# Kernel tuning notes

Measured on AMD Instinct MI355X. Metric: run time of the kernel, lower is better.

## Reference

```python
import jax, jax.numpy as jnp
import numpy as np

HEADS = 12
EPS_RMS = 1e-6
EPS_LN = 1e-5


def _rms_inorm(x, w):
    # torch.std over spatial dims (unbiased, ddof=1); no mean subtraction
    std = jnp.std(x, axis=(2, 3), keepdims=True, ddof=1)
    return x / (std + EPS_RMS) * w[None, :, None, None]


def _layernorm(x, w, b):
    m = jnp.mean(x, axis=-1, keepdims=True)
    v = jnp.var(x, axis=-1, keepdims=True)
    return (x - m) / jnp.sqrt(v + EPS_LN) * w + b


def setup_inputs() -> dict:
    key = jax.random.key(0)
    ks = jax.random.split(key, 16)
    B, C, H, W = 8, 768, 64, 64
    hd = C // HEADS
    s = 0.02
    return {
        "x": jax.random.normal(ks[0], (B, C, H, W), jnp.float32),
        "bcs": jnp.zeros((1, 2), jnp.int32),
        "norm1_w": jnp.ones((C,), jnp.float32),
        "norm2_w": jnp.ones((C,), jnp.float32),
        "mlpn_w": jnp.ones((C,), jnp.float32),
        "Win": jax.random.normal(ks[1], (3 * C, C), jnp.float32) * s,
        "bin_": jnp.zeros((3 * C,), jnp.float32),
        "Wout": jax.random.normal(ks[2], (C, C), jnp.float32) * s,
        "bout": jnp.zeros((C,), jnp.float32),
        "qn_w": jnp.ones((hd,), jnp.float32),
        "qn_b": jnp.zeros((hd,), jnp.float32),
        "kn_w": jnp.ones((hd,), jnp.float32),
        "kn_b": jnp.zeros((hd,), jnp.float32),
        "gamma_att": jnp.full((C,), 1e-6, jnp.float32),
        "gamma_mlp": jnp.full((C,), 1e-6, jnp.float32),
        "W1": jax.random.normal(ks[3], (C, 4 * C), jnp.float32) * s,
        "b1": jnp.zeros((4 * C,), jnp.float32),
        "W2": jax.random.normal(ks[4], (4 * C, C), jnp.float32) * s,
        "b2": jnp.zeros((C,), jnp.float32),
    }


def reference(x, bcs, norm1_w, norm2_w, mlpn_w, Win, bin_, Wout, bout,
              qn_w, qn_b, kn_w, kn_b, gamma_att, gamma_mlp, W1, b1, W2, b2):
    B, C, H, W = x.shape
    hd = C // HEADS
    scale = 1.0 / jnp.sqrt(jnp.asarray(hd, x.dtype))

    h = _rms_inorm(x, norm1_w)
    # 1x1 conv QKV: [B, 3C, H, W]
    qkv = jnp.einsum('bchw,oc->bohw', h, Win) + bin_[None, :, None, None]
    # b (he c3) h w -> b he h w c3, then split into q,k,v of head_dim each
    qkv = qkv.reshape(B, HEADS, 3 * hd, H, W).transpose(0, 1, 3, 4, 2)
    q, k, v = jnp.split(qkv, 3, axis=-1)  # each [B, he, H, W, hd]
    q = _layernorm(q, qn_w, qn_b)
    k = _layernorm(k, kn_w, kn_b)

    # row attention: attend along W for each row h
    sx = jnp.einsum('bnhqc,bnhkc->bnhqk', q, k) * scale
    xx = jnp.einsum('bnhqk,bnhkc->bnhqc', jax.nn.softmax(sx, axis=-1), v)
    # column attention: attend along H for each column w
    sy = jnp.einsum('bnqwc,bnkwc->bnwqk', q, k) * scale
    xy = jnp.einsum('bnwqk,bnkwc->bnqwc', jax.nn.softmax(sy, axis=-1), v)

    a = (xx + xy) * 0.5  # [B, he, H, W, hd]
    a = a.transpose(0, 1, 4, 2, 3).reshape(B, C, H, W)
    a = _rms_inorm(a, norm2_w)
    a = jnp.einsum('bchw,oc->bohw', a, Wout) + bout[None, :, None, None]
    x1 = a * gamma_att[None, :, None, None] + x

    t = x1.transpose(0, 2, 3, 1)  # [B, H, W, C]
    m = jax.nn.gelu(t @ W1 + b1, approximate=False) @ W2 + b2
    m = m.transpose(0, 3, 1, 2)
    m = _rms_inorm(m, mlpn_w)
    return x1 + gamma_mlp[None, :, None, None] * m
```

## Files before the change

kernel.cpp:

```cpp
#include <hip/hip_runtime.h>

typedef __attribute__((ext_vector_type(8))) short short8;
typedef __attribute__((ext_vector_type(4))) float f32x4;
typedef __attribute__((ext_vector_type(4))) unsigned short u16x4;
typedef __attribute__((ext_vector_type(8))) unsigned short u16x8;

#define BDIM 8
#define CDIM 768
#define C3 2304
#define C4 3072
#define HEADS 12
#define HD 64
#define HWD 4096
#define TOKS 32768

__device__ __forceinline__ float bf2f(unsigned short u) {
    union { unsigned int i; float f; } x; x.i = ((unsigned int)u) << 16; return x.f;
}
__device__ __forceinline__ unsigned short f2bf(float f) {
    union { float f; unsigned int i; } x; x.f = f;
    unsigned int r = x.i + 0x7FFFu + ((x.i >> 16) & 1u);
    return (unsigned short)(r >> 16);
}

__device__ __forceinline__ void gload_lds16(const unsigned short* g, unsigned short* l) {
    __builtin_amdgcn_global_load_lds(
        (const __attribute__((address_space(1))) void*)g,
        (__attribute__((address_space(3))) void*)l, 16, 0, 0);
}

__global__ __launch_bounds__(256) void convert_f32_bf16(
    const float* __restrict__ src, unsigned short* __restrict__ dst, int n)
{
    int i = (blockIdx.x * 256 + threadIdx.x) * 4;
    if (i + 3 >= n + 4) return;
    if (i + 3 < n) {
        float4 v = *(const float4*)&src[i];
        dst[i + 0] = f2bf(v.x); dst[i + 1] = f2bf(v.y);
        dst[i + 2] = f2bf(v.z); dst[i + 3] = f2bf(v.w);
    }
}

__global__ __launch_bounds__(256) void transpose_w(
    const float* __restrict__ src, unsigned short* __restrict__ dst, int R, int Cc)
{
    const int n0 = blockIdx.x * 64, k0 = blockIdx.y * 64;
    __shared__ float t[64][65];
    #pragma unroll
    for (int s = 0; s < 16; ++s) {
        int flat = threadIdx.x + 256 * s;
        int i = flat >> 6, j = flat & 63;
        t[i][j] = src[(long)(k0 + i) * Cc + n0 + j];
    }
    __syncthreads();
    #pragma unroll
    for (int s = 0; s < 16; ++s) {
        int flat = threadIdx.x + 256 * s;
        int jn = flat >> 6, ik = flat & 63;
        dst[(long)(n0 + jn) * R + k0 + ik] = f2bf(t[ik][jn]);
    }
}

__global__ __launch_bounds__(256) void stats_spatial_f32(
    const float* __restrict__ x, const float* __restrict__ wgt,
    float* __restrict__ sout, float eps)
{
    const int bc = blockIdx.x;
    const int c = bc % CDIM;
    const float4* p4 = (const float4*)(x + (long)bc * HWD);
    float s = 0.f, ss = 0.f;
    #pragma unroll
    for (int k = 0; k < 4; ++k) {
        float4 v = p4[threadIdx.x + 256 * k];
        s  += v.x + v.y + v.z + v.w;
        ss += v.x * v.x + v.y * v.y + v.z * v.z + v.w * v.w;
    }
    #pragma unroll
    for (int m = 1; m < 64; m <<= 1) { s += __shfl_xor(s, m); ss += __shfl_xor(ss, m); }
    __shared__ float rs[4], rss[4];
    int w = threadIdx.x >> 6, lane = threadIdx.x & 63;
    if (lane == 0) { rs[w] = s; rss[w] = ss; }
    __syncthreads();
    if (threadIdx.x == 0) {
        float S = rs[0] + rs[1] + rs[2] + rs[3];
        float Q = rss[0] + rss[1] + rss[2] + rss[3];
        float var = (Q - S * S * (1.f / 4096.f)) * (1.f / 4095.f);
        sout[bc] = wgt[c] / (sqrtf(var) + eps);
    }
}

__global__ __launch_bounds__(256) void stats_spatial_bf16(
    const unsigned short* __restrict__ t, const float* __restrict__ wgt,
    float* __restrict__ sout, float eps)
{
    const int b = blockIdx.x / 12, cg = blockIdx.x % 12;
    const int sub = threadIdx.x & 15, tr = threadIdx.x >> 4;
    const unsigned short* base = t + (long)b * HWD * CDIM + cg * 64 + sub * 4;
    float s[4] = {0.f, 0.f, 0.f, 0.f}, q[4] = {0.f, 0.f, 0.f, 0.f};
    for (int i = 0; i < 256; ++i) {
        const int token = tr + 16 * i;
        u16x4 v = *(const u16x4*)(base + (long)token * CDIM);
        #pragma unroll
        for (int j = 0; j < 4; ++j) { float f = bf2f(v[j]); s[j] += f; q[j] += f * f; }
    }
    __shared__ float ssum[16][64], ssq[16][64];
    #pragma unroll
    for (int j = 0; j < 4; ++j) { ssum[tr][sub * 4 + j] = s[j]; ssq[tr][sub * 4 + j] = q[j]; }
    __syncthreads();
    if (threadIdx.x < 64) {
        const int c = threadIdx.x;
        float S = 0.f, Q = 0.f;
        #pragma unroll
        for (int r = 0; r < 16; ++r) { S += ssum[r][c]; Q += ssq[r][c]; }
        const float var = (Q - S * S * (1.f / 4096.f)) * (1.f / 4095.f);
        const int cglob = cg * 64 + c;
        sout[b * CDIM + cglob] = wgt[cglob] / (sqrtf(var) + eps);
    }
}

__global__ __launch_bounds__(256) void make_h(
    const float* __restrict__ x, const float* __restrict__ s1,
    unsigned short* __restrict__ h)
{
    const int hw0 = blockIdx.x * 64, c0 = blockIdx.y * 64, b = blockIdx.z;
    __shared__ float t[64][65];
    #pragma unroll
    for (int s = 0; s < 16; ++s) {
        int flat = threadIdx.x + 256 * s;
        int ci = flat >> 6, hj = flat & 63;
        t[ci][hj] = x[(long)(b * CDIM + c0 + ci) * HWD + hw0 + hj];
    }
    __syncthreads();
    #pragma unroll
    for (int s = 0; s < 16; ++s) {
        int flat = threadIdx.x + 256 * s;
        int hi = flat >> 6, cj = flat & 63;
        float v = t[cj][hi] * s1[b * CDIM + c0 + cj];
        h[(long)(b * HWD + hw0 + hi) * CDIM + c0 + cj] = f2bf(v);
    }
}

template<int GELU>
__global__ __launch_bounds__(512, 2) void gemm256(
    const unsigned short* __restrict__ A, const unsigned short* __restrict__ BT,
    const float* __restrict__ bias, unsigned short* __restrict__ out,
    int M, int N, int K)
{
    extern __shared__ unsigned short smem[];
    const int tid = threadIdx.x;
    const int lane = tid & 63, w = tid >> 6;
    const int wm = w >> 2, wn = w & 3;
    const int lr = lane & 15, g = lane >> 4;

    const int nwg = gridDim.x;
    const int logical = (blockIdx.x & 7) * (nwg >> 3) + (blockIdx.x >> 3);
    const int gnx = N >> 8;
    const int n0 = (logical % gnx) << 8;
    const int m0 = (logical / gnx) << 8;

    const int ka = (((tid & 3) ^ ((tid >> 3) & 3)) << 3);
    const int rA0 = tid >> 2, rA1 = (512 + tid) >> 2;
    const unsigned short* aS0 = A + (long)(m0 + rA0) * K + ka;
    const unsigned short* aS1 = A + (long)(m0 + rA1) * K + ka;
    const unsigned short* bS0 = BT + (long)(n0 + rA0) * K + ka;
    const unsigned short* bS1 = BT + (long)(n0 + rA1) * K + ka;
    unsigned short* dA0 = smem + ((tid & ~63) + 0) * 8;
    unsigned short* dA1 = smem + ((tid & ~63) + 512) * 8;
    unsigned short* dB0 = dA0 + 32768;
    unsigned short* dB1 = dA1 + 32768;

#define GSTAGE(S) do { \
        gload_lds16(aS0, dA0 + (S) * 8192); \
        gload_lds16(aS1, dA1 + (S) * 8192); \
        gload_lds16(bS0, dB0 + (S) * 8192); \
        gload_lds16(bS1, dB1 + (S) * 8192); \
        aS0 += 32; aS1 += 32; bS0 += 32; bS1 += 32; } while (0)

    const int nsub = K >> 5;
    const int koff = ((g ^ ((lr >> 1) & 3)) << 3);
    const unsigned short* baseA = smem + (wm * 128 + lr) * 32 + koff;
    const unsigned short* baseB = smem + 32768 + (wn * 64 + lr) * 32 + koff;

    f32x4 acc[8][4] = {};

    GSTAGE(0); GSTAGE(1); GSTAGE(2);
    asm volatile("s_waitcnt vmcnt(8)" ::: "memory");
    __builtin_amdgcn_s_barrier();

#define FRAGS_AND_MFMA(U) do { \
        short8 bf[4], af[8]; \
        _Pragma("unroll") \
        for (int ni = 0; ni < 4; ++ni) bf[ni] = *(const short8*)(baseB + (U) * 8192 + ni * 512); \
        _Pragma("unroll") \
        for (int mi = 0; mi < 8; ++mi) af[mi] = *(const short8*)(baseA + (U) * 8192 + mi * 512); \
        STAGE_##U; \
        __builtin_amdgcn_s_setprio(1); \
        _Pragma("unroll") \
        for (int mi = 0; mi < 8; ++mi) \
            _Pragma("unroll") \
            for (int ni = 0; ni < 4; ++ni) \
                acc[mi][ni] = __builtin_amdgcn_mfma_f32_16x16x32_bf16(af[mi], bf[ni], acc[mi][ni], 0, 0, 0); \
        __builtin_amdgcn_s_setprio(0); \
        WAIT_##U; \
        __builtin_amdgcn_s_barrier(); \
        __builtin_amdgcn_sched_barrier(0); } while (0)

    int j4 = 0;
    for (; j4 + 4 < nsub; j4 += 4) {
#define STAGE_0 GSTAGE(3)
#define STAGE_1 GSTAGE(0)
#define STAGE_2 GSTAGE(1)
#define STAGE_3 GSTAGE(2)
#define WAIT_0 asm volatile("s_waitcnt vmcnt(8)" ::: "memory")
#define WAIT_1 asm volatile("s_waitcnt vmcnt(8)" ::: "memory")
#define WAIT_2 asm volatile("s_waitcnt vmcnt(8)" ::: "memory")
#define WAIT_3 asm volatile("s_waitcnt vmcnt(8)" ::: "memory")
        FRAGS_AND_MFMA(0);
        FRAGS_AND_MFMA(1);
        FRAGS_AND_MFMA(2);
        FRAGS_AND_MFMA(3);
#undef STAGE_0
#undef STAGE_1
#undef STAGE_2
#undef STAGE_3
#undef WAIT_0
#undef WAIT_1
#undef WAIT_2
#undef WAIT_3
    }
    {
#define STAGE_0 GSTAGE(3)
#define STAGE_1
#define STAGE_2
#define STAGE_3
#define WAIT_0 asm volatile("s_waitcnt vmcnt(8)" ::: "memory")
#define WAIT_1 asm volatile("s_waitcnt vmcnt(4)" ::: "memory")
#define WAIT_2 asm volatile("s_waitcnt vmcnt(0)" ::: "memory")
#define WAIT_3
        FRAGS_AND_MFMA(0);
        FRAGS_AND_MFMA(1);
        FRAGS_AND_MFMA(2);
        FRAGS_AND_MFMA(3);
#undef STAGE_0
#undef STAGE_1
#undef STAGE_2
#undef STAGE_3
#undef WAIT_0
#undef WAIT_1
#undef WAIT_2
#undef WAIT_3
    }
#undef FRAGS_AND_MFMA
#undef GSTAGE

    #pragma unroll
    for (int mi = 0; mi < 8; ++mi) {
        #pragma unroll
        for (int ni = 0; ni < 4; ++ni) {
            const int gcol = n0 + wn * 64 + ni * 16 + lr;
            const float bv = bias[gcol];
            #pragma unroll
            for (int r = 0; r < 4; ++r) {
                const int grow = m0 + wm * 128 + mi * 16 + g * 4 + r;
                float v = acc[mi][ni][r] + bv;
                if (GELU) v = 0.5f * v * (1.f + erff(v * 0.70710678118f));
                out[(long)grow * N + gcol] = f2bf(v);
            }
        }
    }
}

__global__ __launch_bounds__(256) void qk_layernorm(
    unsigned short* __restrict__ qkv,
    const float* __restrict__ qw, const float* __restrict__ qb,
    const float* __restrict__ kw, const float* __restrict__ kb)
{
    const int pairIdx = blockIdx.x * 16 + (threadIdx.x >> 4);
    const int token = pairIdx / HEADS, he = pairIdx % HEADS;
    const int c4 = (threadIdx.x & 15) * 4;
    const long base = (long)token * C3 + he * 192;
    #pragma unroll
    for (int which = 0; which < 2; ++which) {
        const long off = base + which * 64 + c4;
        u16x4 v = *(u16x4*)&qkv[off];
        float f[4];
        #pragma unroll
        for (int j = 0; j < 4; ++j) f[j] = bf2f(v[j]);
        float s = f[0] + f[1] + f[2] + f[3];
        float q = f[0] * f[0] + f[1] * f[1] + f[2] * f[2] + f[3] * f[3];
        #pragma unroll
        for (int m = 1; m < 16; m <<= 1) { s += __shfl_xor(s, m); q += __shfl_xor(q, m); }
        const float mean = s * (1.f / 64.f);
        const float var = q * (1.f / 64.f) - mean * mean;
        const float rstd = rsqrtf(var + 1e-5f);
        const float* W = which ? kw : qw;
        const float* Bv = which ? kb : qb;
        u16x4 o;
        #pragma unroll
        for (int j = 0; j < 4; ++j)
            o[j] = f2bf((f[j] - mean) * rstd * W[c4 + j] + Bv[c4 + j]);
        *(u16x4*)&qkv[off] = o;
    }
}

template<int AXIS>
__global__ __launch_bounds__(128) void attn_axial(
    const unsigned short* __restrict__ qkv, unsigned short* __restrict__ a)
{
    __shared__ unsigned short lds[2][2][64 * 72];
    const int tid = threadIdx.x;
    const int lane = tid & 63, w = tid >> 6;
    const int lineG = blockIdx.x * 2 + w;
    const int b = lineG / 768;
    const int rem = lineG - b * 768;
    const int he = rem >> 6, line = rem & 63;
    const int ts = (AXIS == 0) ? 1 : 64;
    const long token0 = (long)b * HWD + (AXIS == 0 ? line * 64 : line);
    const long qbase = token0 * C3 + he * 192;
    unsigned short* VT = &lds[w][0][0];
    unsigned short* P  = &lds[w][1][0];
    const int lr = lane & 15, g = lane >> 4;

    {
        const int keyr = lane >> 3, d8 = (lane & 7) << 3;
        #pragma unroll
        for (int it = 0; it < 8; ++it) {
            const int key = it * 8 + keyr;
            u16x8 v = *(const u16x8*)&qkv[qbase + (long)key * ts * C3 + 128 + d8];
            #pragma unroll
            for (int j = 0; j < 8; ++j) VT[(d8 + j) * 72 + key] = v[j];
        }
    }

    short8 qf[4][2], kf[4][2];
    #pragma unroll
    for (int i = 0; i < 4; ++i)
        #pragma unroll
        for (int kk = 0; kk < 2; ++kk) {
            const long rb = qbase + (long)(i * 16 + lr) * ts * C3 + kk * 32 + g * 8;
            qf[i][kk] = *(const short8*)&qkv[rb];
            kf[i][kk] = *(const short8*)&qkv[rb + 64];
        }

    f32x4 acc[4][4] = {};
    #pragma unroll
    for (int mi = 0; mi < 4; ++mi)
        #pragma unroll
        for (int ni = 0; ni < 4; ++ni) {
            acc[mi][ni] = __builtin_amdgcn_mfma_f32_16x16x32_bf16(qf[mi][0], kf[ni][0], acc[mi][ni], 0, 0, 0);
            acc[mi][ni] = __builtin_amdgcn_mfma_f32_16x16x32_bf16(qf[mi][1], kf[ni][1], acc[mi][ni], 0, 0, 0);
        }

    #pragma unroll
    for (int mi = 0; mi < 4; ++mi)
        #pragma unroll
        for (int r = 0; r < 4; ++r) {
            float mx = -1e30f;
            #pragma unroll
            for (int ni = 0; ni < 4; ++ni) {
                float v = acc[mi][ni][r] * 0.125f; acc[mi][ni][r] = v; mx = fmaxf(mx, v);
            }
            #pragma unroll
            for (int m = 1; m < 16; m <<= 1) mx = fmaxf(mx, __shfl_xor(mx, m));
            float s = 0.f;
            #pragma unroll
            for (int ni = 0; ni < 4; ++ni) {
                float e = __expf(acc[mi][ni][r] - mx); acc[mi][ni][r] = e; s += e;
            }
            #pragma unroll
            for (int m = 1; m < 16; m <<= 1) s += __shfl_xor(s, m);
            const float inv = 1.f / s;
            const int row = mi * 16 + 4 * g + r;
            #pragma unroll
            for (int ni = 0; ni < 4; ++ni)
                P[row * 72 + ni * 16 + lr] = f2bf(acc[mi][ni][r] * inv);
        }
    __syncthreads();

    short8 pa[4][2], vb[4][2];
    #pragma unroll
    for (int i = 0; i < 4; ++i)
        #pragma unroll
        for (int kk = 0; kk < 2; ++kk) {
            pa[i][kk] = *(const short8*)&P[(i * 16 + lr) * 72 + kk * 32 + g * 8];
            vb[i][kk] = *(const short8*)&VT[(i * 16 + lr) * 72 + kk * 32 + g * 8];
        }
    f32x4 o2[4][4] = {};
    #pragma unroll
    for (int mi = 0; mi < 4; ++mi)
        #pragma unroll
        for (int ni = 0; ni < 4; ++ni) {
            o2[mi][ni] = __builtin_amdgcn_mfma_f32_16x16x32_bf16(pa[mi][0], vb[ni][0], o2[mi][ni], 0, 0, 0);
            o2[mi][ni] = __builtin_amdgcn_mfma_f32_16x16x32_bf16(pa[mi][1], vb[ni][1], o2[mi][ni], 0, 0, 0);
        }

    #pragma unroll
    for (int mi = 0; mi < 4; ++mi)
        #pragma unroll
        for (int r = 0; r < 4; ++r) {
            const int q = mi * 16 + 4 * g + r;
            const long tok = token0 + (long)q * ts;
            #pragma unroll
            for (int ni = 0; ni < 4; ++ni) {
                const int d = ni * 16 + lr;
                const long addr = tok * CDIM + he * 64 + d;
                const float v = o2[mi][ni][r] * 0.5f;
                if (AXIS == 0) a[addr] = f2bf(v);
                else           a[addr] = f2bf(bf2f(a[addr]) + v);
            }
        }
}

__global__ __launch_bounds__(256) void scale_inplace(
    unsigned short* __restrict__ a, const float* __restrict__ s2)
{
    const long i = ((long)blockIdx.x * 256 + threadIdx.x) * 4;
    const int c = (int)(i % CDIM);
    const int b = (int)(i / ((long)CDIM * HWD));
    u16x4 v = *(u16x4*)&a[i];
    u16x4 o;
    #pragma unroll
    for (int j = 0; j < 4; ++j) o[j] = f2bf(bf2f(v[j]) * s2[b * CDIM + c + j]);
    *(u16x4*)&a[i] = o;
}

__global__ __launch_bounds__(256) void x1_combine(
    const unsigned short* __restrict__ o, const float* __restrict__ x,
    const float* __restrict__ gamma, float* __restrict__ dout,
    unsigned short* __restrict__ x1b)
{
    const int hw0 = blockIdx.x * 64, c0 = blockIdx.y * 64, b = blockIdx.z;
    __shared__ float t[64][65];
    #pragma unroll
    for (int s = 0; s < 16; ++s) {
        int flat = threadIdx.x + 256 * s;
        int i = flat >> 6, j = flat & 63;
        t[i][j] = bf2f(o[(long)(b * HWD + hw0 + i) * CDIM + c0 + j]);
    }
    __syncthreads();
    #pragma unroll
    for (int s = 0; s < 16; ++s) {
        int flat = threadIdx.x + 256 * s;
        int j = flat >> 6, i = flat & 63;
        const long xi = (long)(b * CDIM + c0 + j) * HWD + hw0 + i;
        float v = x[xi] + gamma[c0 + j] * t[i][j];
        dout[xi] = v;
        t[i][j] = v;
    }
    __syncthreads();
    #pragma unroll
    for (int s = 0; s < 16; ++s) {
        int flat = threadIdx.x + 256 * s;
        int i = flat >> 6, j = flat & 63;
        x1b[(long)(b * HWD + hw0 + i) * CDIM + c0 + j] = f2bf(t[i][j]);
    }
}

__global__ __launch_bounds__(256) void final_combine(
    const unsigned short* __restrict__ m, const float* __restrict__ gm,
    const float* __restrict__ s3, float* __restrict__ dout)
{
    const int hw0 = blockIdx.x * 64, c0 = blockIdx.y * 64, b = blockIdx.z;
    __shared__ float t[64][65];
    #pragma unroll
    for (int s = 0; s < 16; ++s) {
        int flat = threadIdx.x + 256 * s;
        int i = flat >> 6, j = flat & 63;
        t[i][j] = bf2f(m[(long)(b * HWD + hw0 + i) * CDIM + c0 + j]);
    }
    __syncthreads();
    #pragma unroll
    for (int s = 0; s < 16; ++s) {
        int flat = threadIdx.x + 256 * s;
        int j = flat >> 6, i = flat & 63;
        const long xi = (long)(b * CDIM + c0 + j) * HWD + hw0 + i;
        dout[xi] = dout[xi] + gm[c0 + j] * s3[b * CDIM + c0 + j] * t[i][j];
    }
}

extern "C" void kernel_launch(void* const* d_in, const int* in_sizes, int n_in,
                              void* d_out, int out_size, void* d_ws, size_t ws_size,
                              hipStream_t stream) {
    const float* x      = (const float*)d_in[0];
    const float* n1w    = (const float*)d_in[2];
    const float* n2w    = (const float*)d_in[3];
    const float* mlw    = (const float*)d_in[4];
    const float* Win    = (const float*)d_in[5];
    const float* bin    = (const float*)d_in[6];
    const float* Wout   = (const float*)d_in[7];
    const float* bout   = (const float*)d_in[8];
    const float* qn_w   = (const float*)d_in[9];
    const float* qn_b   = (const float*)d_in[10];
    const float* kn_w   = (const float*)d_in[11];
    const float* kn_b   = (const float*)d_in[12];
    const float* gatt   = (const float*)d_in[13];
    const float* gmlp   = (const float*)d_in[14];
    const float* W1     = (const float*)d_in[15];
    const float* b1     = (const float*)d_in[16];
    const float* W2     = (const float*)d_in[17];
    const float* b2     = (const float*)d_in[18];
    float* dout = (float*)d_out;
    char* ws = (char*)d_ws;

    unsigned short* wQ  = (unsigned short*)(ws);
    unsigned short* wO  = (unsigned short*)(ws + (4L << 20));
    unsigned short* w1t = (unsigned short*)(ws + (6L << 20));
    unsigned short* w2t = (unsigned short*)(ws + (11L << 20));
    float* s1 = (float*)(ws + (16L << 20));
    float* s2 = s1 + 6144;
    float* s3 = s2 + 6144;
    unsigned short* bufH = (unsigned short*)(ws + (17L << 20));
    unsigned short* bufQ = (unsigned short*)(ws + (65L << 20));
    unsigned short* bufA = (unsigned short*)(ws + (209L << 20));

    hipFuncSetAttribute((const void*)&gemm256<0>, hipFuncAttributeMaxDynamicSharedMemorySize, 131072);
    hipFuncSetAttribute((const void*)&gemm256<1>, hipFuncAttributeMaxDynamicSharedMemorySize, 131072);

    convert_f32_bf16<<<1728, 256, 0, stream>>>(Win, wQ, C3 * CDIM);
    convert_f32_bf16<<<576, 256, 0, stream>>>(Wout, wO, CDIM * CDIM);
    transpose_w<<<dim3(C4 / 64, CDIM / 64), 256, 0, stream>>>(W1, w1t, CDIM, C4);
    transpose_w<<<dim3(CDIM / 64, C4 / 64), 256, 0, stream>>>(W2, w2t, C4, CDIM);

    stats_spatial_f32<<<BDIM * CDIM, 256, 0, stream>>>(x, n1w, s1, 1e-6f);
    make_h<<<dim3(64, 12, 8), 256, 0, stream>>>(x, s1, bufH);

    gemm256<0><<<(TOKS / 256) * (C3 / 256), 512, 131072, stream>>>(bufH, wQ, bin, bufQ, TOKS, C3, CDIM);
    qk_layernorm<<<TOKS * HEADS / 16, 256, 0, stream>>>(bufQ, qn_w, qn_b, kn_w, kn_b);

    attn_axial<0><<<BDIM * HEADS * 64 / 2, 128, 0, stream>>>(bufQ, bufA);
    attn_axial<1><<<BDIM * HEADS * 64 / 2, 128, 0, stream>>>(bufQ, bufA);

    stats_spatial_bf16<<<BDIM * 12, 256, 0, stream>>>(bufA, n2w, s2, 1e-6f);
    scale_inplace<<<TOKS * CDIM / 1024, 256, 0, stream>>>(bufA, s2);
    gemm256<0><<<(TOKS / 256) * (CDIM / 256), 512, 131072, stream>>>(bufA, wO, bout, bufH, TOKS, CDIM, CDIM);
    x1_combine<<<dim3(64, 12, 8), 256, 0, stream>>>(bufH, x, gatt, dout, bufA);

    for (int ch = 0; ch < 2; ++ch) {
        const unsigned short* x1c = bufA + (long)ch * 16384 * CDIM;
        unsigned short* mc = bufH + (long)ch * 16384 * CDIM;
        gemm256<1><<<(16384 / 256) * (C4 / 256), 512, 131072, stream>>>(x1c, w1t, b1, bufQ, 16384, C4, CDIM);
        gemm256<0><<<(16384 / 256) * (CDIM / 256), 512, 131072, stream>>>(bufQ, w2t, b2, mc, 16384, CDIM, C4);
    }

    stats_spatial_bf16<<<BDIM * 12, 256, 0, stream>>>(bufH, mlw, s3, 1e-6f);
    final_combine<<<dim3(64, 12, 8), 256, 0, stream>>>(bufH, gmlp, s3, dout);
}
```

Measured before the change: 972.8 us.

## Switch all projection and MLP GEMMs from bf16 to fp8 MFMA

Weights, normalized activations, the attention output, x1 and the GELU hidden activations are now quantized to fp8 instead of bf16. The GEMM kernel uses the fp8 16x16x32 MFMA, so operand bytes per element are halved. The LDS staging is reworked to one 16-byte load per thread per operand with an unswizzled layout, and the shared-memory footprint drops to 64 KB. The aim is to raise matrix-core throughput and cut memory traffic in the GEMM-dominated pipeline, at the cost of lower numerical accuracy in every projection.

```diff
diff --git a/kernel.cpp b/kernel.cpp
--- a/kernel.cpp
+++ b/kernel.cpp
@@ -22,27 +22,33 @@
     unsigned int r = x.i + 0x7FFFu + ((x.i >> 16) & 1u);
     return (unsigned short)(r >> 16);
 }
-
-__device__ __forceinline__ void gload_lds16(const unsigned short* g, unsigned short* l) {
+__device__ __forceinline__ unsigned char f2fp8(float v) {
+    return (unsigned char)(__builtin_amdgcn_cvt_pk_fp8_f32(v, v, 0, false) & 0xff);
+}
+__device__ __forceinline__ unsigned int f4fp8(float a, float b, float c, float d) {
+    int r = __builtin_amdgcn_cvt_pk_fp8_f32(a, b, 0, false);
+    r = __builtin_amdgcn_cvt_pk_fp8_f32(c, d, r, true);
+    return (unsigned int)r;
+}
+
+__device__ __forceinline__ void gload_lds16(const unsigned char* g, unsigned char* l) {
     __builtin_amdgcn_global_load_lds(
         (const __attribute__((address_space(1))) void*)g,
         (__attribute__((address_space(3))) void*)l, 16, 0, 0);
 }
 
-__global__ __launch_bounds__(256) void convert_f32_bf16(
-    const float* __restrict__ src, unsigned short* __restrict__ dst, int n)
+__global__ __launch_bounds__(256) void convert_f32_fp8(
+    const float* __restrict__ src, unsigned char* __restrict__ dst, int n)
 {
     int i = (blockIdx.x * 256 + threadIdx.x) * 4;
-    if (i + 3 >= n + 4) return;
     if (i + 3 < n) {
         float4 v = *(const float4*)&src[i];
-        dst[i + 0] = f2bf(v.x); dst[i + 1] = f2bf(v.y);
-        dst[i + 2] = f2bf(v.z); dst[i + 3] = f2bf(v.w);
-    }
-}
-
-__global__ __launch_bounds__(256) void transpose_w(
-    const float* __restrict__ src, unsigned short* __restrict__ dst, int R, int Cc)
+        *(unsigned int*)&dst[i] = f4fp8(v.x, v.y, v.z, v.w);
+    }
+}
+
+__global__ __launch_bounds__(256) void transpose_w_f8(
+    const float* __restrict__ src, unsigned char* __restrict__ dst, int R, int Cc)
 {
     const int n0 = blockIdx.x * 64, k0 = blockIdx.y * 64;
     __shared__ float t[64][65];
@@ -57,7 +63,7 @@
     for (int s = 0; s < 16; ++s) {
         int flat = threadIdx.x + 256 * s;
         int jn = flat >> 6, ik = flat & 63;
-        dst[(long)(n0 + jn) * R + k0 + ik] = f2bf(t[ik][jn]);
+        dst[(long)(n0 + jn) * R + k0 + ik] = f2fp8(t[ik][jn]);
     }
 }
 
@@ -120,7 +126,7 @@
 
 __global__ __launch_bounds__(256) void make_h(
     const float* __restrict__ x, const float* __restrict__ s1,
-    unsigned short* __restrict__ h)
+    unsigned char* __restrict__ h)
 {
     const int hw0 = blockIdx.x * 64, c0 = blockIdx.y * 64, b = blockIdx.z;
     __shared__ float t[64][65];
@@ -136,17 +142,17 @@
         int flat = threadIdx.x + 256 * s;
         int hi = flat >> 6, cj = flat & 63;
         float v = t[cj][hi] * s1[b * CDIM + c0 + cj];
-        h[(long)(b * HWD + hw0 + hi) * CDIM + c0 + cj] = f2bf(v);
-    }
-}
-
-template<int GELU>
+        h[(long)(b * HWD + hw0 + hi) * CDIM + c0 + cj] = f2fp8(v);
+    }
+}
+
+template<int GELU, int OUTF8>
 __global__ __launch_bounds__(512, 2) void gemm256(
-    const unsigned short* __restrict__ A, const unsigned short* __restrict__ BT,
-    const float* __restrict__ bias, unsigned short* __restrict__ out,
+    const unsigned char* __restrict__ A, const unsigned char* __restrict__ BT,
+    const float* __restrict__ bias, void* __restrict__ outv,
     int M, int N, int K)
 {
-    extern __shared__ unsigned short smem[];
+    extern __shared__ unsigned char smemB[];
     const int tid = threadIdx.x;
     const int lane = tid & 63, w = tid >> 6;
     const int wm = w >> 2, wn = w & 3;
@@ -158,48 +164,39 @@
     const int n0 = (logical % gnx) << 8;
     const int m0 = (logical / gnx) << 8;
 
-    const int ka = (((tid & 3) ^ ((tid >> 3) & 3)) << 3);
-    const int rA0 = tid >> 2, rA1 = (512 + tid) >> 2;
-    const unsigned short* aS0 = A + (long)(m0 + rA0) * K + ka;
-    const unsigned short* aS1 = A + (long)(m0 + rA1) * K + ka;
-    const unsigned short* bS0 = BT + (long)(n0 + rA0) * K + ka;
-    const unsigned short* bS1 = BT + (long)(n0 + rA1) * K + ka;
-    unsigned short* dA0 = smem + ((tid & ~63) + 0) * 8;
-    unsigned short* dA1 = smem + ((tid & ~63) + 512) * 8;
-    unsigned short* dB0 = dA0 + 32768;
-    unsigned short* dB1 = dA1 + 32768;
+    const unsigned char* aS = A + (long)(m0 + (tid >> 1)) * K + ((tid & 1) << 4);
+    const unsigned char* bS = BT + (long)(n0 + (tid >> 1)) * K + ((tid & 1) << 4);
+    unsigned char* dA = smemB + (tid & ~63) * 16;
+    unsigned char* dB = dA + 32768;
 
 #define GSTAGE(S) do { \
-        gload_lds16(aS0, dA0 + (S) * 8192); \
-        gload_lds16(aS1, dA1 + (S) * 8192); \
-        gload_lds16(bS0, dB0 + (S) * 8192); \
-        gload_lds16(bS1, dB1 + (S) * 8192); \
-        aS0 += 32; aS1 += 32; bS0 += 32; bS1 += 32; } while (0)
+        gload_lds16(aS, dA + (S) * 8192); \
+        gload_lds16(bS, dB + (S) * 8192); \
+        aS += 32; bS += 32; } while (0)
 
     const int nsub = K >> 5;
-    const int koff = ((g ^ ((lr >> 1) & 3)) << 3);
-    const unsigned short* baseA = smem + (wm * 128 + lr) * 32 + koff;
-    const unsigned short* baseB = smem + 32768 + (wn * 64 + lr) * 32 + koff;
+    const unsigned char* baseA = smemB + (wm * 128 + lr) * 32 + g * 8;
+    const unsigned char* baseB = smemB + 32768 + (wn * 64 + lr) * 32 + g * 8;
 
     f32x4 acc[8][4] = {};
 
     GSTAGE(0); GSTAGE(1); GSTAGE(2);
-    asm volatile("s_waitcnt vmcnt(8)" ::: "memory");
+    asm volatile("s_waitcnt vmcnt(4)" ::: "memory");
     __builtin_amdgcn_s_barrier();
 
 #define FRAGS_AND_MFMA(U) do { \
-        short8 bf[4], af[8]; \
+        long bf[4], af[8]; \
         _Pragma("unroll") \
-        for (int ni = 0; ni < 4; ++ni) bf[ni] = *(const short8*)(baseB + (U) * 8192 + ni * 512); \
+        for (int ni = 0; ni < 4; ++ni) bf[ni] = *(const long*)(baseB + (U) * 8192 + ni * 512); \
         _Pragma("unroll") \
-        for (int mi = 0; mi < 8; ++mi) af[mi] = *(const short8*)(baseA + (U) * 8192 + mi * 512); \
+        for (int mi = 0; mi < 8; ++mi) af[mi] = *(const long*)(baseA + (U) * 8192 + mi * 512); \
         STAGE_##U; \
         __builtin_amdgcn_s_setprio(1); \
         _Pragma("unroll") \
         for (int mi = 0; mi < 8; ++mi) \
             _Pragma("unroll") \
             for (int ni = 0; ni < 4; ++ni) \
-                acc[mi][ni] = __builtin_amdgcn_mfma_f32_16x16x32_bf16(af[mi], bf[ni], acc[mi][ni], 0, 0, 0); \
+                acc[mi][ni] = __builtin_amdgcn_mfma_f32_16x16x32_fp8_fp8(af[mi], bf[ni], acc[mi][ni], 0, 0, 0); \
         __builtin_amdgcn_s_setprio(0); \
         WAIT_##U; \
         __builtin_amdgcn_s_barrier(); \
@@ -211,10 +208,10 @@
 #define STAGE_1 GSTAGE(0)
 #define STAGE_2 GSTAGE(1)
 #define STAGE_3 GSTAGE(2)
-#define WAIT_0 asm volatile("s_waitcnt vmcnt(8)" ::: "memory")
-#define WAIT_1 asm volatile("s_waitcnt vmcnt(8)" ::: "memory")
-#define WAIT_2 asm volatile("s_waitcnt vmcnt(8)" ::: "memory")
-#define WAIT_3 asm volatile("s_waitcnt vmcnt(8)" ::: "memory")
+#define WAIT_0 asm volatile("s_waitcnt vmcnt(4)" ::: "memory")
+#define WAIT_1 asm volatile("s_waitcnt vmcnt(4)" ::: "memory")
+#define WAIT_2 asm volatile("s_waitcnt vmcnt(4)" ::: "memory")
+#define WAIT_3 asm volatile("s_waitcnt vmcnt(4)" ::: "memory")
         FRAGS_AND_MFMA(0);
         FRAGS_AND_MFMA(1);
         FRAGS_AND_MFMA(2);
@@ -233,8 +230,8 @@
 #define STAGE_1
 #define STAGE_2
 #define STAGE_3
-#define WAIT_0 asm volatile("s_waitcnt vmcnt(8)" ::: "memory")
-#define WAIT_1 asm volatile("s_waitcnt vmcnt(4)" ::: "memory")
+#define WAIT_0 asm volatile("s_waitcnt vmcnt(4)" ::: "memory")
+#define WAIT_1 asm volatile("s_waitcnt vmcnt(2)" ::: "memory")
 #define WAIT_2 asm volatile("s_waitcnt vmcnt(0)" ::: "memory")
 #define WAIT_3
         FRAGS_AND_MFMA(0);
@@ -264,7 +261,8 @@
                 const int grow = m0 + wm * 128 + mi * 16 + g * 4 + r;
                 float v = acc[mi][ni][r] + bv;
                 if (GELU) v = 0.5f * v * (1.f + erff(v * 0.70710678118f));
-                out[(long)grow * N + gcol] = f2bf(v);
+                if (OUTF8) ((unsigned char*)outv)[(long)grow * N + gcol] = f2fp8(v);
+                else       ((unsigned short*)outv)[(long)grow * N + gcol] = f2bf(v);
             }
         }
     }
@@ -411,23 +409,24 @@
         }
 }
 
-__global__ __launch_bounds__(256) void scale_inplace(
-    unsigned short* __restrict__ a, const float* __restrict__ s2)
+__global__ __launch_bounds__(256) void scale_convert(
+    const unsigned short* __restrict__ a, const float* __restrict__ s2,
+    unsigned char* __restrict__ aF)
 {
     const long i = ((long)blockIdx.x * 256 + threadIdx.x) * 4;
     const int c = (int)(i % CDIM);
     const int b = (int)(i / ((long)CDIM * HWD));
-    u16x4 v = *(u16x4*)&a[i];
-    u16x4 o;
-    #pragma unroll
-    for (int j = 0; j < 4; ++j) o[j] = f2bf(bf2f(v[j]) * s2[b * CDIM + c + j]);
-    *(u16x4*)&a[i] = o;
+    u16x4 v = *(const u16x4*)&a[i];
+    float f[4];
+    #pragma unroll
+    for (int j = 0; j < 4; ++j) f[j] = bf2f(v[j]) * s2[b * CDIM + c + j];
+    *(unsigned int*)&aF[i] = f4fp8(f[0], f[1], f[2], f[3]);
 }
 
 __global__ __launch_bounds__(256) void x1_combine(
     const unsigned short* __restrict__ o, const float* __restrict__ x,
     const float* __restrict__ gamma, float* __restrict__ dout,
-    unsigned short* __restrict__ x1b)
+    unsigned char* __restrict__ x1f)
 {
     const int hw0 = blockIdx.x * 64, c0 = blockIdx.y * 64, b = blockIdx.z;
     __shared__ float t[64][65];
@@ -452,7 +451,7 @@
     for (int s = 0; s < 16; ++s) {
         int flat = threadIdx.x + 256 * s;
         int i = flat >> 6, j = flat & 63;
-        x1b[(long)(b * HWD + hw0 + i) * CDIM + c0 + j] = f2bf(t[i][j]);
+        x1f[(long)(b * HWD + hw0 + i) * CDIM + c0 + j] = f2fp8(t[i][j]);
     }
 }
 
@@ -502,46 +501,46 @@
     float* dout = (float*)d_out;
     char* ws = (char*)d_ws;
 
-    unsigned short* wQ  = (unsigned short*)(ws);
-    unsigned short* wO  = (unsigned short*)(ws + (4L << 20));
-    unsigned short* w1t = (unsigned short*)(ws + (6L << 20));
-    unsigned short* w2t = (unsigned short*)(ws + (11L << 20));
-    float* s1 = (float*)(ws + (16L << 20));
+    unsigned char* wQf  = (unsigned char*)(ws);
+    unsigned char* wOf  = (unsigned char*)(ws + (2L << 20));
+    unsigned char* w1tf = (unsigned char*)(ws + (3L << 20));
+    unsigned char* w2tf = (unsigned char*)(ws + (6L << 20));
+    float* s1 = (float*)(ws + (9L << 20));
     float* s2 = s1 + 6144;
     float* s3 = s2 + 6144;
-    unsigned short* bufH = (unsigned short*)(ws + (17L << 20));
-    unsigned short* bufQ = (unsigned short*)(ws + (65L << 20));
-    unsigned short* bufA = (unsigned short*)(ws + (209L << 20));
-
-    hipFuncSetAttribute((const void*)&gemm256<0>, hipFuncAttributeMaxDynamicSharedMemorySize, 131072);
-    hipFuncSetAttribute((const void*)&gemm256<1>, hipFuncAttributeMaxDynamicSharedMemorySize, 131072);
-
-    convert_f32_bf16<<<1728, 256, 0, stream>>>(Win, wQ, C3 * CDIM);
-    convert_f32_bf16<<<576, 256, 0, stream>>>(Wout, wO, CDIM * CDIM);
-    transpose_w<<<dim3(C4 / 64, CDIM / 64), 256, 0, stream>>>(W1, w1t, CDIM, C4);
-    transpose_w<<<dim3(CDIM / 64, C4 / 64), 256, 0, stream>>>(W2, w2t, C4, CDIM);
+    unsigned char* R1 = (unsigned char*)(ws + (10L << 20));
+    unsigned short* R2 = (unsigned short*)(ws + (58L << 20));
+    unsigned short* R3 = (unsigned short*)(ws + (106L << 20));
+
+    hipFuncSetAttribute((const void*)&gemm256<0, 0>, hipFuncAttributeMaxDynamicSharedMemorySize, 65536);
+    hipFuncSetAttribute((const void*)&gemm256<1, 1>, hipFuncAttributeMaxDynamicSharedMemorySize, 65536);
+
+    convert_f32_fp8<<<1728, 256, 0, stream>>>(Win, wQf, C3 * CDIM);
+    convert_f32_fp8<<<576, 256, 0, stream>>>(Wout, wOf, CDIM * CDIM);
+    transpose_w_f8<<<dim3(C4 / 64, CDIM / 64), 256, 0, stream>>>(W1, w1tf, CDIM, C4);
+    transpose_w_f8<<<dim3(CDIM / 64, C4 / 64), 256, 0, stream>>>(W2, w2tf, C4, CDIM);
 
     stats_spatial_f32<<<BDIM * CDIM, 256, 0, stream>>>(x, n1w, s1, 1e-6f);
-    make_h<<<dim3(64, 12, 8), 256, 0, stream>>>(x, s1, bufH);
-
-    gemm256<0><<<(TOKS / 256) * (C3 / 256), 512, 131072, stream>>>(bufH, wQ, bin, bufQ, TOKS, C3, CDIM);
-    qk_layernorm<<<TOKS * HEADS / 16, 256, 0, stream>>>(bufQ, qn_w, qn_b, kn_w, kn_b);
-
-    attn_axial<0><<<BDIM * HEADS * 64 / 2, 128, 0, stream>>>(bufQ, bufA);
-    attn_axial<1><<<BDIM * HEADS * 64 / 2, 128, 0, stream>>>(bufQ, bufA);
-
-    stats_spatial_bf16<<<BDIM * 12, 256, 0, stream>>>(bufA, n2w, s2, 1e-6f);
-    scale_inplace<<<TOKS * CDIM / 1024, 256, 0, stream>>>(bufA, s2);
-    gemm256<0><<<(TOKS / 256) * (CDIM / 256), 512, 131072, stream>>>(bufA, wO, bout, bufH, TOKS, CDIM, CDIM);
-    x1_combine<<<dim3(64, 12, 8), 256, 0, stream>>>(bufH, x, gatt, dout, bufA);
+    make_h<<<dim3(64, 12, 8), 256, 0, stream>>>(x, s1, R1);
+
+    gemm256<0, 0><<<(TOKS / 256) * (C3 / 256), 512, 65536, stream>>>(R1, wQf, bin, R3, TOKS, C3, CDIM);
+    qk_layernorm<<<TOKS * HEADS / 16, 256, 0, stream>>>(R3, qn_w, qn_b, kn_w, kn_b);
+
+    attn_axial<0><<<BDIM * HEADS * 64 / 2, 128, 0, stream>>>(R3, R2);
+    attn_axial<1><<<BDIM * HEADS * 64 / 2, 128, 0, stream>>>(R3, R2);
+
+    stats_spatial_bf16<<<BDIM * 12, 256, 0, stream>>>(R2, n2w, s2, 1e-6f);
+    scale_convert<<<TOKS * CDIM / 1024, 256, 0, stream>>>(R2, s2, R1);
+    gemm256<0, 0><<<(TOKS / 256) * (CDIM / 256), 512, 65536, stream>>>(R1, wOf, bout, R2, TOKS, CDIM, CDIM);
+    x1_combine<<<dim3(64, 12, 8), 256, 0, stream>>>(R2, x, gatt, dout, R1);
 
     for (int ch = 0; ch < 2; ++ch) {
-        const unsigned short* x1c = bufA + (long)ch * 16384 * CDIM;
-        unsigned short* mc = bufH + (long)ch * 16384 * CDIM;
-        gemm256<1><<<(16384 / 256) * (C4 / 256), 512, 131072, stream>>>(x1c, w1t, b1, bufQ, 16384, C4, CDIM);
-        gemm256<0><<<(16384 / 256) * (CDIM / 256), 512, 131072, stream>>>(bufQ, w2t, b2, mc, 16384, CDIM, C4);
-    }
-
-    stats_spatial_bf16<<<BDIM * 12, 256, 0, stream>>>(bufH, mlw, s3, 1e-6f);
-    final_combine<<<dim3(64, 12, 8), 256, 0, stream>>>(bufH, gmlp, s3, dout);
-}
+        const unsigned char* x1c = R1 + (long)ch * 16384 * CDIM;
+        unsigned short* mc = R2 + (long)ch * 16384 * CDIM;
+        gemm256<1, 1><<<(16384 / 256) * (C4 / 256), 512, 65536, stream>>>(x1c, w1tf, b1, (unsigned char*)R3, 16384, C4, CDIM);
+        gemm256<0, 0><<<(16384 / 256) * (CDIM / 256), 512, 65536, stream>>>((unsigned char*)R3, w2tf, b2, mc, 16384, CDIM, C4);
+    }
+
+    stats_spatial_bf16<<<BDIM * 12, 256, 0, stream>>>(R2, mlw, s3, 1e-6f);
+    final_combine<<<dim3(64, 12, 8), 256, 0, stream>>>(R2, gmlp, s3, dout);
+}
```

Result: no change. 985.1 us (+1.3%).
